# Optimization experiments

Hardware: AMD Instinct MI355X
Metric: run time of the kernel (lower is better)

## Reference

```python
import jax, jax.numpy as jnp
import numpy as np

B, L, D, H, KV = 2, 2048, 2048, 16, 4
K = D // H  # head dim = 128
ROPE_BASE = 10000.0


def _rope_tables(seq_len, dim):
    inv_freq = 1.0 / (ROPE_BASE ** (jnp.arange(0, dim, 2, dtype=jnp.float32) / dim))
    t = jnp.arange(seq_len, dtype=jnp.float32)
    freqs = jnp.outer(t, inv_freq)  # [L, dim/2]
    return jnp.cos(freqs), jnp.sin(freqs)


def _apply_rope(x, cos, sin):
    # x: [B, h, L, K]; interleaved-pair rotation, matching torch stack+flatten
    x1 = x[..., ::2]
    x2 = x[..., 1::2]
    c = cos[None, None, :, :]
    s = sin[None, None, :, :]
    o1 = x1 * c - x2 * s
    o2 = x1 * s + x2 * c
    return jnp.stack((o1, o2), axis=-1).reshape(x.shape)


def setup_inputs() -> dict:
    key = jax.random.key(0)
    ks = jax.random.split(key, 5)
    scale = D ** -0.5
    return {
        "x": jax.random.normal(ks[0], (B, L, D), jnp.float32),
        "wq": jax.random.normal(ks[1], (D, D), jnp.float32) * scale,
        "wk": jax.random.normal(ks[2], (KV * K, D), jnp.float32) * scale,
        "wv": jax.random.normal(ks[3], (KV * K, D), jnp.float32) * scale,
        "wo": jax.random.normal(ks[4], (D, D), jnp.float32) * scale,
    }


def reference(x, wq, wk, wv, wo):
    Bx, Lx, Dx = x.shape
    # projections (nn.Linear: y = x @ W.T)
    q = (x @ wq.T).reshape(Bx, Lx, H, K).transpose(0, 2, 1, 3)   # [B,H,L,K]
    k = (x @ wk.T).reshape(Bx, Lx, KV, K).transpose(0, 2, 1, 3)  # [B,KV,L,K]
    v = (x @ wv.T).reshape(Bx, Lx, KV, K).transpose(0, 2, 1, 3)
    cos, sin = _rope_tables(Lx, K)
    q = _apply_rope(q, cos, sin)
    k = _apply_rope(k, cos, sin)
    # GQA: repeat_interleave KV heads to H heads
    rep = H // KV
    k = jnp.repeat(k, rep, axis=1)
    v = jnp.repeat(v, rep, axis=1)
    scores = jnp.einsum('bhqd,bhkd->bhqk', q, k) / jnp.sqrt(jnp.float32(K))
    causal = jnp.tril(jnp.ones((Lx, Lx), dtype=bool))
    scores = jnp.where(causal[None, None], scores, jnp.finfo(scores.dtype).min)
    attn = jax.nn.softmax(scores, axis=-1)
    out = jnp.einsum('bhqk,bhkd->bhqd', attn, v)
    out = out.transpose(0, 2, 1, 3).reshape(Bx, Lx, Dx)
    return out @ wo.T
```

## Files before the change

### kernel.cpp

```cpp
#include <hip/hip_runtime.h>
#include <stdint.h>

#define DEV static __device__ __forceinline__

typedef __attribute__((ext_vector_type(8))) short s16x8;
typedef __attribute__((ext_vector_type(4))) short s16x4;
typedef __attribute__((ext_vector_type(4))) float f32x4;

constexpr int BB = 2, LL = 2048, DD = 2048, NH = 16, NKV = 4, HD = 128;
constexpr int Mrows = BB * LL;
constexpr int NQKV = DD + 2 * NKV * HD;

DEV ushort f2bf(float f){
  union { float f; uint32_t u; } v; v.f = f;
  uint32_t u = v.u;
  u += 0x7fffu + ((u >> 16) & 1u);
  return (ushort)(u >> 16);
}
DEV float bf2f(ushort h){
  union { uint32_t u; float f; } v; v.u = ((uint32_t)h) << 16;
  return v.f;
}

DEV f32x4 mfma32(s16x8 a, s16x8 b, f32x4 c){
  return __builtin_amdgcn_mfma_f32_16x16x32_bf16(a, b, c, 0, 0, 0);
}
DEV f32x4 mfma16(s16x4 a, s16x4 b, f32x4 c){
#if __has_builtin(__builtin_amdgcn_mfma_f32_16x16x16bf16_1k)
  return __builtin_amdgcn_mfma_f32_16x16x16bf16_1k(a, b, c, 0, 0, 0);
#else
  asm volatile("v_mfma_f32_16x16x16_bf16 %0, %1, %2, %0" : "+v"(c) : "v"(a), "v"(b));
  return c;
#endif
}

DEV float vmax4(f32x4 v){ return fmaxf(fmaxf(v[0], v[1]), fmaxf(v[2], v[3])); }
DEV float vsum4(f32x4 v){ return (v[0] + v[1]) + (v[2] + v[3]); }

__global__ void cvt_all_kernel(const float* __restrict__ x, const float* __restrict__ wq,
                               const float* __restrict__ wk, const float* __restrict__ wv,
                               const float* __restrict__ wo,
                               ushort* __restrict__ xb, ushort* __restrict__ wqkv,
                               ushort* __restrict__ wob){
  constexpr int C0 = Mrows * DD / 4;
  constexpr int C1 = C0 + DD * DD / 4;
  constexpr int C2 = C1 + NKV * HD * DD / 4;
  constexpr int C3 = C2 + NKV * HD * DD / 4;
  constexpr int C4 = C3 + DD * DD / 4;
  int stride = gridDim.x * blockDim.x;
  for (int i = blockIdx.x * blockDim.x + threadIdx.x; i < C4; i += stride){
    const float* src; ushort* dst; int j;
    if (i < C0){ src = x;  dst = xb;                              j = i; }
    else if (i < C1){ src = wq; dst = wqkv;                       j = i - C0; }
    else if (i < C2){ src = wk; dst = wqkv + (size_t)DD * DD;     j = i - C1; }
    else if (i < C3){ src = wv; dst = wqkv + (size_t)(DD + NKV*HD) * DD; j = i - C2; }
    else { src = wo; dst = wob;                                   j = i - C3; }
    float4 v = reinterpret_cast<const float4*>(src)[j];
    ushort4 o = make_ushort4(f2bf(v.x), f2bf(v.y), f2bf(v.z), f2bf(v.w));
    reinterpret_cast<ushort4*>(dst)[j] = o;
  }
}

__global__ void rope_table_kernel(float* __restrict__ cosT, float* __restrict__ sinT){
  int i = blockIdx.x * blockDim.x + threadIdx.x;
  if (i >= LL * 64) return;
  int l = i >> 6, f = i & 63;
  float inv = __expf(-logf(10000.f) * (float)f / 64.f);
  float ang = (float)l * inv;
  float s, c;
  sincosf(ang, &s, &c);
  cosT[i] = c; sinT[i] = s;
}

__global__ void rope_qk_kernel(ushort* __restrict__ q, ushort* __restrict__ k,
                               const float* __restrict__ cosT, const float* __restrict__ sinT){
  constexpr int TQ = BB * NH * LL * 16;
  constexpr int TK = BB * NKV * LL * 16;
  int idx = blockIdx.x * blockDim.x + threadIdx.x;
  if (idx >= TQ + TK) return;
  ushort* t; float scale; int id;
  if (idx < TQ){ t = q; id = idx; scale = 0.08838834764831845f; }
  else { t = k; id = idx - TQ; scale = 1.0f; }
  int c = id & 15;
  int l = (id >> 4) & (LL - 1);
  s16x8 v = *reinterpret_cast<const s16x8*>(t + (size_t)id * 8);
  int fb = (l << 6) + c * 4;
  s16x8 o;
  #pragma unroll
  for (int j = 0; j < 4; ++j){
    float x1 = bf2f((ushort)v[2*j]);
    float x2 = bf2f((ushort)v[2*j+1]);
    float co = cosT[fb + j], si = sinT[fb + j];
    o[2*j]   = (short)f2bf((x1 * co - x2 * si) * scale);
    o[2*j+1] = (short)f2bf((x1 * si + x2 * co) * scale);
  }
  *reinterpret_cast<s16x8*>(t + (size_t)id * 8) = o;
}

DEV void g2l16(const void* g, void* l){
  __builtin_amdgcn_global_load_lds((__attribute__((address_space(1))) void*)(void*)g,
                                   (__attribute__((address_space(3))) void*)l, 16, 0, 0);
}

__global__ __launch_bounds__(256) void gemm_qkv_kernel(const ushort* __restrict__ A,
    const ushort* __restrict__ W, ushort* __restrict__ qo, ushort* __restrict__ ko,
    ushort* __restrict__ vo)
{
  __shared__ ushort Asm[128 * 32];
  __shared__ ushort Bsm[128 * 32];
  const int tid = threadIdx.x;
  const int lane = tid & 63;
  const int wr = tid >> 7;
  const int wc = (tid >> 6) & 1;
  const int lr = lane & 15, lg = lane >> 4;
  const int id = blockIdx.x;
  const int nid = (id & 7) * 96 + (id >> 3);
  const int bx = nid >> 5;
  const int by = nid & 31;
  const int brow = by * 128, bcol = bx * 128;

  f32x4 acc[4][4] = {};

  for (int kb = 0; kb < DD; kb += 32){
    #pragma unroll
    for (int it = 0; it < 2; ++it){
      int seg = it * 256 + tid;
      int row = seg >> 2, sc = seg & 3;
      g2l16(A + (size_t)(brow + row) * DD + kb + sc * 8, &Asm[seg * 8]);
    }
    #pragma unroll
    for (int it = 0; it < 2; ++it){
      int seg = it * 256 + tid;
      int row = seg >> 2, sc = seg & 3;
      g2l16(W + (size_t)(bcol + row) * DD + kb + sc * 8, &Bsm[seg * 8]);
    }
    __syncthreads();
    s16x8 af[4], bfr[4];
    #pragma unroll
    for (int m = 0; m < 4; ++m)
      af[m] = *reinterpret_cast<const s16x8*>(&Asm[(wr*64 + m*16 + lr)*32 + lg*8]);
    #pragma unroll
    for (int n = 0; n < 4; ++n)
      bfr[n] = *reinterpret_cast<const s16x8*>(&Bsm[(wc*64 + n*16 + lr)*32 + lg*8]);
    #pragma unroll
    for (int m = 0; m < 4; ++m)
      #pragma unroll
      for (int n = 0; n < 4; ++n)
        acc[m][n] = mfma32(af[m], bfr[n], acc[m][n]);
    __syncthreads();
  }

  #pragma unroll
  for (int m = 0; m < 4; ++m)
    #pragma unroll
    for (int n = 0; n < 4; ++n)
      #pragma unroll
      for (int r = 0; r < 4; ++r){
        int row = brow + wr*64 + m*16 + lg*4 + r;
        int col = bcol + wc*64 + n*16 + lr;
        int b = row >> 11, l = row & (LL - 1);
        ushort bv = f2bf(acc[m][n][r]);
        if (col < DD){
          qo[(((size_t)(b * NH + (col >> 7))) * LL + l) * HD + (col & 127)] = bv;
        } else if (col < DD + NKV * HD){
          int c = col - DD;
          ko[(((size_t)(b * NKV + (c >> 7))) * LL + l) * HD + (c & 127)] = bv;
        } else {
          int c = col - DD - NKV * HD;
          vo[(((size_t)(b * NKV + (c >> 7))) * HD + (c & 127)) * LL + l] = bv;
        }
      }
}

__global__ __launch_bounds__(256) void gemm_o_kernel(const ushort* __restrict__ A,
    const ushort* __restrict__ W, float* __restrict__ outp)
{
  __shared__ ushort Asm[128 * 32];
  __shared__ ushort Bsm[128 * 32];
  const int tid = threadIdx.x;
  const int lane = tid & 63;
  const int wr = tid >> 7;
  const int wc = (tid >> 6) & 1;
  const int lr = lane & 15, lg = lane >> 4;
  const int id = blockIdx.x;
  const int nid = (id & 7) * 64 + (id >> 3);
  const int bx = nid >> 5;
  const int by = nid & 31;
  const int brow = by * 128, bcol = bx * 128;

  f32x4 acc[4][4] = {};

  for (int kb = 0; kb < DD; kb += 32){
    #pragma unroll
    for (int it = 0; it < 2; ++it){
      int seg = it * 256 + tid;
      int row = seg >> 2, sc = seg & 3;
      g2l16(A + (size_t)(brow + row) * DD + kb + sc * 8, &Asm[seg * 8]);
    }
    #pragma unroll
    for (int it = 0; it < 2; ++it){
      int seg = it * 256 + tid;
      int row = seg >> 2, sc = seg & 3;
      g2l16(W + (size_t)(bcol + row) * DD + kb + sc * 8, &Bsm[seg * 8]);
    }
    __syncthreads();
    s16x8 af[4], bfr[4];
    #pragma unroll
    for (int m = 0; m < 4; ++m)
      af[m] = *reinterpret_cast<const s16x8*>(&Asm[(wr*64 + m*16 + lr)*32 + lg*8]);
    #pragma unroll
    for (int n = 0; n < 4; ++n)
      bfr[n] = *reinterpret_cast<const s16x8*>(&Bsm[(wc*64 + n*16 + lr)*32 + lg*8]);
    #pragma unroll
    for (int m = 0; m < 4; ++m)
      #pragma unroll
      for (int n = 0; n < 4; ++n)
        acc[m][n] = mfma32(af[m], bfr[n], acc[m][n]);
    __syncthreads();
  }

  #pragma unroll
  for (int m = 0; m < 4; ++m)
    #pragma unroll
    for (int n = 0; n < 4; ++n)
      #pragma unroll
      for (int r = 0; r < 4; ++r){
        int row = brow + wr*64 + m*16 + lg*4 + r;
        int col = bcol + wc*64 + n*16 + lr;
        outp[(size_t)row * DD + col] = acc[m][n][r];
      }
}

template<int NQ>
DEV void tile_step(const ushort* __restrict__ Ks, const ushort* __restrict__ Vs,
                   const s16x8 (*qf)[4], f32x4 (*of)[8], float* mrun, float* lrun,
                   const int* qrow, int jb, int lr, int lg)
{
  f32x4 s[4][NQ];
  #pragma unroll
  for (int kt = 0; kt < 4; ++kt)
    #pragma unroll
    for (int q = 0; q < NQ; ++q) s[kt][q] = (f32x4){0.f, 0.f, 0.f, 0.f};

  __builtin_amdgcn_s_setprio(1);
  #pragma unroll
  for (int kk = 0; kk < 4; ++kk)
    #pragma unroll
    for (int kt = 0; kt < 4; ++kt){
      s16x8 kf = *reinterpret_cast<const s16x8*>(
          &Ks[((kt*16 + lr) << 7) + (((kk*4 + lg) ^ (lr & 7)) << 3)]);
      #pragma unroll
      for (int q = 0; q < NQ; ++q)
        s[kt][q] = mfma32(kf, qf[q][kk], s[kt][q]);
    }
  __builtin_amdgcn_s_setprio(0);

  #pragma unroll
  for (int q = 0; q < NQ; ++q)
    if (jb + 63 > qrow[q]){
      int qg = qrow[q] + lr;
      #pragma unroll
      for (int kt = 0; kt < 4; ++kt){
        int kvg = jb + kt*16 + lg*4;
        #pragma unroll
        for (int r = 0; r < 4; ++r)
          if (kvg + r > qg) s[kt][q][r] = -1e30f;
      }
    }

  float mx[NQ];
  #pragma unroll
  for (int q = 0; q < NQ; ++q){
    mx[q] = fmaxf(fmaxf(vmax4(s[0][q]), vmax4(s[1][q])),
                  fmaxf(vmax4(s[2][q]), vmax4(s[3][q])));
    mx[q] = fmaxf(mx[q], __shfl_xor(mx[q], 16, 64));
    mx[q] = fmaxf(mx[q], __shfl_xor(mx[q], 32, 64));
  }
  int small = 1;
  #pragma unroll
  for (int q = 0; q < NQ; ++q) small &= (mx[q] <= mrun[q] + 8.f);
  if (!__all(small)){
    #pragma unroll
    for (int q = 0; q < NQ; ++q){
      float mn = fmaxf(mrun[q], mx[q]);
      float fac = __expf(mrun[q] - mn);
      mrun[q] = mn;
      lrun[q] *= fac;
      #pragma unroll
      for (int f = 0; f < 8; ++f) of[q][f] *= fac;
    }
  }
  float ps[NQ];
  #pragma unroll
  for (int q = 0; q < NQ; ++q) ps[q] = 0.f;
  #pragma unroll
  for (int kt = 0; kt < 4; ++kt)
    #pragma unroll
    for (int q = 0; q < NQ; ++q){
      #pragma unroll
      for (int r = 0; r < 4; ++r)
        s[kt][q][r] = __expf(s[kt][q][r] - mrun[q]);
      ps[q] += vsum4(s[kt][q]);
    }
  #pragma unroll
  for (int q = 0; q < NQ; ++q){
    ps[q] += __shfl_xor(ps[q], 16, 64);
    ps[q] += __shfl_xor(ps[q], 32, 64);
    lrun[q] += ps[q];
  }
  s16x4 pb[4][NQ];
  #pragma unroll
  for (int kt = 0; kt < 4; ++kt)
    #pragma unroll
    for (int q = 0; q < NQ; ++q){
      s16x4 pv;
      #pragma unroll
      for (int r = 0; r < 4; ++r) pv[r] = (short)f2bf(s[kt][q][r]);
      pb[kt][q] = pv;
    }
  __builtin_amdgcn_s_setprio(1);
  #pragma unroll
  for (int f = 0; f < 8; ++f)
    #pragma unroll
    for (int kt = 0; kt < 4; ++kt){
      s16x4 va = *reinterpret_cast<const s16x4*>(
          &Vs[((f*16 + lr) << 6) + (((2*kt + (lg >> 1)) ^ (lr & 7)) << 3) + ((lg & 1) << 2)]);
      #pragma unroll
      for (int q = 0; q < NQ; ++q)
        of[q][f] = mfma16(va, pb[kt][q], of[q][f]);
    }
  __builtin_amdgcn_s_setprio(0);
}

__global__ __launch_bounds__(256) void attn_kernel(const ushort* __restrict__ Q,
    const ushort* __restrict__ Kg, const ushort* __restrict__ VTg, ushort* __restrict__ O)
{
  __shared__ ushort Ksm[2][64 * 128];
  __shared__ ushort Vsm[2][128 * 64];
  const int tid = threadIdx.x;
  const int w = tid >> 6, lane = tid & 63;
  const int lr = lane & 15, lg = lane >> 4;
  const int id = blockIdx.x;
  const int nid = (id & 7) * 64 + (id >> 3);
  const int pair = nid & 15;
  const int bh = nid >> 4;
  const int b = bh >> 4, h = bh & 15, kvh = h >> 2;
  const size_t qoff = (size_t)bh * LL * HD;
  const size_t koff = (size_t)(b * NKV + kvh) * LL * HD;
  const size_t voff = (size_t)(b * NKV + kvh) * HD * LL;
  const int qrow[2] = { pair*64 + w*16, (31 - pair)*64 + w*16 };
  const int nt  = 32 - pair;
  const int ntA = pair + 1;

  s16x8 qf[2][4];
  #pragma unroll
  for (int qt = 0; qt < 2; ++qt)
    #pragma unroll
    for (int kk = 0; kk < 4; ++kk)
      qf[qt][kk] = *reinterpret_cast<const s16x8*>(
          &Q[qoff + (size_t)(qrow[qt] + lr) * HD + kk*32 + lg*8]);

  f32x4 of[2][8] = {};
  float mrun[2] = {-1e30f, -1e30f}, lrun[2] = {0.f, 0.f};

  auto STAGE = [&](int buf, int jb){
    #pragma unroll
    for (int it = 0; it < 4; ++it){
      int chunk = it * 256 + tid;
      int r = chunk >> 4, c = chunk & 15;
      g2l16(Kg + koff + (size_t)(jb + r) * HD + ((c ^ (r & 7)) << 3), &Ksm[buf][chunk << 3]);
    }
    #pragma unroll
    for (int it = 0; it < 4; ++it){
      int chunk = it * 256 + tid;
      int r = chunk >> 3, c = chunk & 7;
      g2l16(VTg + voff + (size_t)r * LL + jb + ((c ^ (r & 7)) << 3), &Vsm[buf][chunk << 3]);
    }
  };
  STAGE(0, 0);

  for (int t = 0; t < nt; ++t){
    const int jb = t << 6, cur = t & 1;
    __syncthreads();
    if (t + 1 < nt) STAGE(cur ^ 1, (t + 1) << 6);
    if (t < ntA)
      tile_step<2>(Ksm[cur], Vsm[cur], qf, of, mrun, lrun, qrow, jb, lr, lg);
    else
      tile_step<1>(Ksm[cur], Vsm[cur], qf + 1, of + 1, mrun + 1, lrun + 1, qrow + 1, jb, lr, lg);
  }

  #pragma unroll
  for (int qt = 0; qt < 2; ++qt){
    float inv = 1.0f / lrun[qt];
    #pragma unroll
    for (int f = 0; f < 8; ++f)
      #pragma unroll
      for (int r = 0; r < 4; ++r){
        int row = qrow[qt] + lr;
        int col = h * HD + f*16 + lg*4 + r;
        O[((size_t)b * LL + row) * DD + col] = f2bf(of[qt][f][r] * inv);
      }
  }
}

extern "C" void kernel_launch(void* const* d_in, const int* in_sizes, int n_in,
                              void* d_out, int out_size, void* d_ws, size_t ws_size,
                              hipStream_t stream)
{
  const float* x  = (const float*)d_in[0];
  const float* wq = (const float*)d_in[1];
  const float* wk = (const float*)d_in[2];
  const float* wv = (const float*)d_in[3];
  const float* wo = (const float*)d_in[4];
  float* out = (float*)d_out;

  char* p = (char*)d_ws;
  auto alloc = [&](size_t bytes) -> void* {
    void* r = (void*)p; p += (bytes + 255) & ~(size_t)255; return r;
  };
  ushort* xb    = (ushort*)alloc((size_t)Mrows * DD * 2);
  ushort* wqkvb = (ushort*)alloc((size_t)NQKV * DD * 2);
  ushort* wob   = (ushort*)alloc((size_t)DD * DD * 2);
  ushort* qws   = (ushort*)alloc((size_t)BB * NH * LL * HD * 2);
  ushort* kws   = (ushort*)alloc((size_t)BB * NKV * LL * HD * 2);
  ushort* vws   = (ushort*)alloc((size_t)BB * NKV * LL * HD * 2);
  ushort* aows  = (ushort*)alloc((size_t)Mrows * DD * 2);
  float*  cosT  = (float*)alloc((size_t)LL * 64 * 4);
  float*  sinT  = (float*)alloc((size_t)LL * 64 * 4);

  hipLaunchKernelGGL(cvt_all_kernel, dim3(2048), dim3(256), 0, stream,
                     x, wq, wk, wv, wo, xb, wqkvb, wob);
  hipLaunchKernelGGL(rope_table_kernel, dim3((LL*64)/256), dim3(256), 0, stream, cosT, sinT);

  hipLaunchKernelGGL(gemm_qkv_kernel, dim3(768), dim3(256), 0, stream,
                     xb, wqkvb, qws, kws, vws);

  {
    constexpr int tot = BB*NH*LL*16 + BB*NKV*LL*16;
    hipLaunchKernelGGL(rope_qk_kernel, dim3(tot/256), dim3(256), 0, stream,
                       qws, kws, cosT, sinT);
  }

  hipLaunchKernelGGL(attn_kernel, dim3(512), dim3(256), 0, stream,
                     qws, kws, vws, aows);

  hipLaunchKernelGGL(gemm_o_kernel, dim3(512), dim3(256), 0, stream,
                     aows, wob, out);
}
```

Baseline: 397.0 us.

## Replace both GEMMs with a pipelined 256x256-tile double-buffered kernel

```diff
diff --git a/kernel.cpp b/kernel.cpp
--- a/kernel.cpp
+++ b/kernel.cpp
@@ -102,132 +102,103 @@
                                    (__attribute__((address_space(3))) void*)l, 16, 0, 0);
 }
 
-__global__ __launch_bounds__(256) void gemm_qkv_kernel(const ushort* __restrict__ A,
-    const ushort* __restrict__ W, ushort* __restrict__ qo, ushort* __restrict__ ko,
-    ushort* __restrict__ vo)
+#define GPHASE(DB, KK, MH, SDB, SKH, SB, ST, VM) { \
+    const ushort* As_ = Asm + ((DB)*2 + (KK)) * 8192 + wm * 128 * 32; \
+    const ushort* Bs_ = Bsm + ((DB)*2 + (KK)) * 8192 + wn * 64 * 32; \
+    s16x8 af_[4], bf_[4]; \
+    _Pragma("unroll") \
+    for (int i_ = 0; i_ < 4; ++i_) \
+      af_[i_] = *(const s16x8*)&As_[(((MH)*4 + i_) * 16 + lr) * 32 + lg * 8]; \
+    _Pragma("unroll") \
+    for (int n_ = 0; n_ < 4; ++n_) \
+      bf_[n_] = *(const s16x8*)&Bs_[(n_ * 16 + lr) * 32 + lg * 8]; \
+    STG(SDB, SKH, SB, ST); \
+    if (VM) asm volatile("s_waitcnt vmcnt(4)" ::: "memory"); \
+    __builtin_amdgcn_s_barrier(); \
+    __builtin_amdgcn_s_setprio(1); \
+    _Pragma("unroll") \
+    for (int i_ = 0; i_ < 4; ++i_) \
+      _Pragma("unroll") \
+      for (int n_ = 0; n_ < 4; ++n_) \
+        acc[(MH)*4 + i_][n_] = mfma32(af_[i_], bf_[n_], acc[(MH)*4 + i_][n_]); \
+    __builtin_amdgcn_s_setprio(0); \
+    __builtin_amdgcn_s_barrier(); \
+  }
+
+template<int MODE>
+__global__ __launch_bounds__(512, 2) void gemm256_kernel(const ushort* __restrict__ A,
+    const ushort* __restrict__ W, float* __restrict__ fout, ushort* __restrict__ qo,
+    ushort* __restrict__ ko, ushort* __restrict__ vo)
 {
-  __shared__ ushort Asm[128 * 32];
-  __shared__ ushort Bsm[128 * 32];
+  extern __shared__ ushort smem[];
+  ushort* Asm = smem;
+  ushort* Bsm = smem + 32768;
   const int tid = threadIdx.x;
-  const int lane = tid & 63;
-  const int wr = tid >> 7;
-  const int wc = (tid >> 6) & 1;
+  const int w = tid >> 6, lane = tid & 63;
   const int lr = lane & 15, lg = lane >> 4;
-  const int id = blockIdx.x;
-  const int nid = (id & 7) * 96 + (id >> 3);
-  const int bx = nid >> 5;
-  const int by = nid & 31;
-  const int brow = by * 128, bcol = bx * 128;
-
-  f32x4 acc[4][4] = {};
-
-  for (int kb = 0; kb < DD; kb += 32){
-    #pragma unroll
-    for (int it = 0; it < 2; ++it){
-      int seg = it * 256 + tid;
-      int row = seg >> 2, sc = seg & 3;
-      g2l16(A + (size_t)(brow + row) * DD + kb + sc * 8, &Asm[seg * 8]);
-    }
-    #pragma unroll
-    for (int it = 0; it < 2; ++it){
-      int seg = it * 256 + tid;
-      int row = seg >> 2, sc = seg & 3;
-      g2l16(W + (size_t)(bcol + row) * DD + kb + sc * 8, &Bsm[seg * 8]);
-    }
-    __syncthreads();
-    s16x8 af[4], bfr[4];
-    #pragma unroll
-    for (int m = 0; m < 4; ++m)
-      af[m] = *reinterpret_cast<const s16x8*>(&Asm[(wr*64 + m*16 + lr)*32 + lg*8]);
-    #pragma unroll
-    for (int n = 0; n < 4; ++n)
-      bfr[n] = *reinterpret_cast<const s16x8*>(&Bsm[(wc*64 + n*16 + lr)*32 + lg*8]);
-    #pragma unroll
-    for (int m = 0; m < 4; ++m)
-      #pragma unroll
-      for (int n = 0; n < 4; ++n)
-        acc[m][n] = mfma32(af[m], bfr[n], acc[m][n]);
-    __syncthreads();
-  }
-
-  #pragma unroll
-  for (int m = 0; m < 4; ++m)
-    #pragma unroll
-    for (int n = 0; n < 4; ++n)
+  const int wm = w >> 2, wn = w & 3;
+  const int cpx = (int)gridDim.x >> 3;
+  const int id = (int)blockIdx.x;
+  const int nid = (id & 7) * cpx + (id >> 3);
+  const int bx = nid >> 4, by = nid & 15;
+  const int brow = by * 256, bcol = bx * 256;
+
+  const ushort* gA = A + (size_t)(brow + w*32 + (lane >> 2)) * 2048 + (lane & 3) * 8;
+  const ushort* gW = W + (size_t)(bcol + w*32 + (lane >> 2)) * 2048 + (lane & 3) * 8;
+  const int ldsOff = w * 1024 + lane * 8;
+
+  f32x4 acc[8][4] = {};
+
+  auto STG = [&](int db, int kh, int isB, int tile){
+    const ushort* g = (isB ? gW : gA) + tile * 64 + kh * 32;
+    ushort* l = (isB ? Bsm : Asm) + (db*2 + kh) * 8192 + ldsOff;
+    g2l16(g, l);
+    g2l16(g + 16 * 2048, l + 512);
+  };
+
+  STG(0,0,0,0); STG(0,0,1,0); STG(0,1,0,0); STG(0,1,1,0); STG(1,0,0,1); STG(1,0,1,1);
+  asm volatile("s_waitcnt vmcnt(4)" ::: "memory");
+  __builtin_amdgcn_s_barrier();
+
+  for (int it = 0; it < 16; ++it){
+    const int t  = 2 * it;
+    const int t2 = (t + 2 < 32) ? t + 2 : 31;
+    const int t3 = (t + 3 < 32) ? t + 3 : 31;
+    GPHASE(0,0,0, 1,1,0, t+1, 0);
+    GPHASE(0,0,1, 1,1,1, t+1, 0);
+    GPHASE(0,1,0, 0,0,0, t2,  0);
+    GPHASE(0,1,1, 0,0,1, t2,  1);
+    GPHASE(1,0,0, 0,1,0, t2,  0);
+    GPHASE(1,0,1, 0,1,1, t2,  0);
+    GPHASE(1,1,0, 1,0,0, t3,  0);
+    GPHASE(1,1,1, 1,0,1, t3,  1);
+  }
+  asm volatile("s_waitcnt vmcnt(0)" ::: "memory");
+
+  #pragma unroll
+  for (int mf = 0; mf < 8; ++mf)
+    #pragma unroll
+    for (int nf = 0; nf < 4; ++nf)
       #pragma unroll
       for (int r = 0; r < 4; ++r){
-        int row = brow + wr*64 + m*16 + lg*4 + r;
-        int col = bcol + wc*64 + n*16 + lr;
-        int b = row >> 11, l = row & (LL - 1);
-        ushort bv = f2bf(acc[m][n][r]);
-        if (col < DD){
-          qo[(((size_t)(b * NH + (col >> 7))) * LL + l) * HD + (col & 127)] = bv;
-        } else if (col < DD + NKV * HD){
-          int c = col - DD;
-          ko[(((size_t)(b * NKV + (c >> 7))) * LL + l) * HD + (c & 127)] = bv;
+        int row = brow + wm*128 + mf*16 + lg*4 + r;
+        int col = bcol + wn*64 + nf*16 + lr;
+        float v = acc[mf][nf][r];
+        if (MODE == 0){
+          fout[(size_t)row * DD + col] = v;
         } else {
-          int c = col - DD - NKV * HD;
-          vo[(((size_t)(b * NKV + (c >> 7))) * HD + (c & 127)) * LL + l] = bv;
+          int b = row >> 11, l = row & (LL - 1);
+          ushort bv = f2bf(v);
+          if (col < DD){
+            qo[(((size_t)(b * NH + (col >> 7))) * LL + l) * HD + (col & 127)] = bv;
+          } else if (col < DD + NKV * HD){
+            int c = col - DD;
+            ko[(((size_t)(b * NKV + (c >> 7))) * LL + l) * HD + (c & 127)] = bv;
+          } else {
+            int c = col - DD - NKV * HD;
+            vo[(((size_t)(b * NKV + (c >> 7))) * HD + (c & 127)) * LL + l] = bv;
+          }
         }
-      }
-}
-
-__global__ __launch_bounds__(256) void gemm_o_kernel(const ushort* __restrict__ A,
-    const ushort* __restrict__ W, float* __restrict__ outp)
-{
-  __shared__ ushort Asm[128 * 32];
-  __shared__ ushort Bsm[128 * 32];
-  const int tid = threadIdx.x;
-  const int lane = tid & 63;
-  const int wr = tid >> 7;
-  const int wc = (tid >> 6) & 1;
-  const int lr = lane & 15, lg = lane >> 4;
-  const int id = blockIdx.x;
-  const int nid = (id & 7) * 64 + (id >> 3);
-  const int bx = nid >> 5;
-  const int by = nid & 31;
-  const int brow = by * 128, bcol = bx * 128;
-
-  f32x4 acc[4][4] = {};
-
-  for (int kb = 0; kb < DD; kb += 32){
-    #pragma unroll
-    for (int it = 0; it < 2; ++it){
-      int seg = it * 256 + tid;
-      int row = seg >> 2, sc = seg & 3;
-      g2l16(A + (size_t)(brow + row) * DD + kb + sc * 8, &Asm[seg * 8]);
-    }
-    #pragma unroll
-    for (int it = 0; it < 2; ++it){
-      int seg = it * 256 + tid;
-      int row = seg >> 2, sc = seg & 3;
-      g2l16(W + (size_t)(bcol + row) * DD + kb + sc * 8, &Bsm[seg * 8]);
-    }
-    __syncthreads();
-    s16x8 af[4], bfr[4];
-    #pragma unroll
-    for (int m = 0; m < 4; ++m)
-      af[m] = *reinterpret_cast<const s16x8*>(&Asm[(wr*64 + m*16 + lr)*32 + lg*8]);
-    #pragma unroll
-    for (int n = 0; n < 4; ++n)
-      bfr[n] = *reinterpret_cast<const s16x8*>(&Bsm[(wc*64 + n*16 + lr)*32 + lg*8]);
-    #pragma unroll
-    for (int m = 0; m < 4; ++m)
-      #pragma unroll
-      for (int n = 0; n < 4; ++n)
-        acc[m][n] = mfma32(af[m], bfr[n], acc[m][n]);
-    __syncthreads();
-  }
-
-  #pragma unroll
-  for (int m = 0; m < 4; ++m)
-    #pragma unroll
-    for (int n = 0; n < 4; ++n)
-      #pragma unroll
-      for (int r = 0; r < 4; ++r){
-        int row = brow + wr*64 + m*16 + lg*4 + r;
-        int col = bcol + wc*64 + n*16 + lr;
-        outp[(size_t)row * DD + col] = acc[m][n][r];
       }
 }
 
@@ -428,12 +399,17 @@
   float*  cosT  = (float*)alloc((size_t)LL * 64 * 4);
   float*  sinT  = (float*)alloc((size_t)LL * 64 * 4);
 
+  hipFuncSetAttribute(reinterpret_cast<const void*>(gemm256_kernel<1>),
+                      hipFuncAttributeMaxDynamicSharedMemorySize, 131072);
+  hipFuncSetAttribute(reinterpret_cast<const void*>(gemm256_kernel<0>),
+                      hipFuncAttributeMaxDynamicSharedMemorySize, 131072);
+
   hipLaunchKernelGGL(cvt_all_kernel, dim3(2048), dim3(256), 0, stream,
                      x, wq, wk, wv, wo, xb, wqkvb, wob);
   hipLaunchKernelGGL(rope_table_kernel, dim3((LL*64)/256), dim3(256), 0, stream, cosT, sinT);
 
-  hipLaunchKernelGGL(gemm_qkv_kernel, dim3(768), dim3(256), 0, stream,
-                     xb, wqkvb, qws, kws, vws);
+  hipLaunchKernelGGL(gemm256_kernel<1>, dim3(192), dim3(512), 131072, stream,
+                     xb, wqkvb, (float*)nullptr, qws, kws, vws);
 
   {
     constexpr int tot = BB*NH*LL*16 + BB*NKV*LL*16;
@@ -444,6 +420,6 @@
   hipLaunchKernelGGL(attn_kernel, dim3(512), dim3(256), 0, stream,
                      qws, kws, vws, aows);
 
-  hipLaunchKernelGGL(gemm_o_kernel, dim3(512), dim3(256), 0, stream,
-                     aows, wob, out);
-}
+  hipLaunchKernelGGL(gemm256_kernel<0>, dim3(128), dim3(512), 131072, stream,
+                     aows, wob, out, (ushort*)nullptr, (ushort*)nullptr, (ushort*)nullptr);
+}
```

Measured after the change: 396.2 us. No clear change (-0.2%).
